# Optimization experiments

Measured on AMD Instinct MI355X. Metric: run time of the kernel, lower is better.

## Reference

```python
import jax, jax.numpy as jnp
import numpy as np

HEADS, DIM_HEAD, C, B, HS, WS = 8, 64, 512, 2, 48, 48


def setup_inputs() -> dict:
    key = jax.random.key(0)
    ks = jax.random.split(key, 9)
    s = 0.02
    return {
        "hidden_states": jax.random.normal(ks[0], (B, C, HS, WS), jnp.float32),
        "Wq": jax.random.normal(ks[1], (HEADS, DIM_HEAD, C), jnp.float32) * s,
        "bq": jax.random.normal(ks[2], (HEADS, DIM_HEAD), jnp.float32) * s,
        "Wk": jax.random.normal(ks[3], (HEADS, DIM_HEAD, C), jnp.float32) * s,
        "bk": jax.random.normal(ks[4], (HEADS, DIM_HEAD), jnp.float32) * s,
        "Wv": jax.random.normal(ks[5], (HEADS, DIM_HEAD, C), jnp.float32) * s,
        "bv": jax.random.normal(ks[6], (HEADS, DIM_HEAD), jnp.float32) * s,
        "Wo": jax.random.normal(ks[7], (C, HEADS * DIM_HEAD), jnp.float32) * s,
        "bo": jax.random.normal(ks[8], (C,), jnp.float32) * s,
    }


def reference(hidden_states, Wq, bq, Wk, bk, Wv, bv, Wo, bo):
    # hidden_states: [B, C, H, W]; per-head 1x1 convs == per-head linear over C.
    b, c, h, w = hidden_states.shape
    hw = h * w
    x = hidden_states.reshape(b, c, hw)  # [B, C, HW]
    # Batched per-head projections (fuses the per-head Conv2d loop).
    q = jnp.einsum('bcs,ndc->bnsd', x, Wq) + bq[None, :, None, :]  # [B, n, HW, d]
    k = jnp.einsum('bcs,ndc->bnsd', x, Wk) + bk[None, :, None, :]
    v = jnp.einsum('bcs,ndc->bnsd', x, Wv) + bv[None, :, None, :]
    scale = 1.0 / jnp.sqrt(jnp.asarray(DIM_HEAD, hidden_states.dtype))
    scores = jnp.einsum('bnqd,bnkd->bnqk', q, k) * scale  # [B, n, HW, HW]
    probs = jax.nn.softmax(scores, axis=-1)
    attn = jnp.einsum('bnqk,bnkd->bnqd', probs, v)  # [B, n, HW, d]
    # concat heads along last dim (matches torch.cat(..., dim=-1))
    attn = attn.transpose(0, 2, 1, 3).reshape(b, hw, HEADS * DIM_HEAD)
    out = attn @ Wo.T + bo  # [B, HW, C] (to_out[0]; to_out[1] dropout = identity)
    out = out.reshape(b, h, w, c).transpose(0, 3, 1, 2)  # [B, C, H, W]
    return out
```

## Files before the change

### kernel.cpp

```cpp
#include <hip/hip_runtime.h>
#include <hip/hip_bf16.h>

#define HEADS 8
#define DHEAD 64
#define CDIM  512
#define SEQ   2304
#define ND    512

typedef unsigned short u16;
typedef unsigned int   u32;
typedef __attribute__((ext_vector_type(8))) short short8;
typedef __attribute__((ext_vector_type(4))) float f32x4;

#define QSCALE 0.18033688011112043f

__device__ __forceinline__ u16 f2bf(float f) {
    union { float f; u32 u; } x; x.f = f;
    u32 r = x.u + 0x7FFFu + ((x.u >> 16) & 1u);
    return (u16)(r >> 16);
}
__device__ __forceinline__ float bf2f(u16 v) {
    union { u32 u; float f; } x; x.u = ((u32)v) << 16; return x.f;
}
__device__ __forceinline__ u32 pkbf(float a, float b) {
    union { float f; u32 u; } x, y; x.f = a; y.f = b;
    return __builtin_amdgcn_perm(y.u + 0x8000u, x.u + 0x8000u, 0x07060302u);
}
__device__ __forceinline__ f32x4 mfma16(short8 a, short8 b, f32x4 c) {
    return __builtin_amdgcn_mfma_f32_16x16x32_bf16(a, b, c, 0, 0, 0);
}
__device__ __forceinline__ void cp16(const void* g, void* l) {
    __builtin_amdgcn_global_load_lds(
        (const __attribute__((address_space(1))) u32*)(uintptr_t)g,
        (__attribute__((address_space(3))) u32*)(u32)(uintptr_t)l,
        16, 0, 0);
}
__device__ __forceinline__ int kperm_inv(int r) {
    return (r & ~0x1C) | ((r & 0x0C) << 1) | ((r & 0x10) >> 2);
}

__global__ void prep_kernel(const float* __restrict__ H,
                            const float* __restrict__ Wq, const float* __restrict__ Wk,
                            const float* __restrict__ Wv, const float* __restrict__ Wo,
                            u16* __restrict__ Wqkv, u16* __restrict__ Wob,
                            u16* __restrict__ X) {
    __shared__ float tile[32][33];
    const int t = threadIdx.x;
    const int bx = blockIdx.x;
    if (bx < 4096) {
        int idx = bx * 256 + t;
        const int N1 = CDIM * ND;
        if (idx < N1)             Wqkv[idx] = f2bf(Wq[idx]);
        else if (idx < 2 * N1)    Wqkv[idx] = f2bf(Wk[idx - N1]);
        else if (idx < 3 * N1)    Wqkv[idx] = f2bf(Wv[idx - 2 * N1]);
        else                      Wob[idx - 3 * N1] = f2bf(Wo[idx - 3 * N1]);
    } else {
        int bb = bx - 4096;
        int st = bb % 72, ct = (bb / 72) % 16, b = bb / (72 * 16);
        int tx = t & 31, ty = t >> 5;
#pragma unroll
        for (int k = 0; k < 4; ++k) {
            int c = ct * 32 + ty + k * 8;
            tile[ty + k * 8][tx] = H[((size_t)b * CDIM + c) * SEQ + st * 32 + tx];
        }
        __syncthreads();
#pragma unroll
        for (int k = 0; k < 4; ++k) {
            int s = st * 32 + ty + k * 8;
            X[((size_t)b * SEQ + s) * CDIM + ct * 32 + tx] = f2bf(tile[tx][ty + k * 8]);
        }
    }
}

__global__ __launch_bounds__(256) void gemm_qkv_kernel(
        const u16* __restrict__ W, const u16* __restrict__ X,
        const float* __restrict__ bq, const float* __restrict__ bk, const float* __restrict__ bv,
        u16* __restrict__ Q, u16* __restrict__ K, u16* __restrict__ V) {
    __shared__ __align__(16) u16 As[128 * 64];
    __shared__ __align__(16) u16 Bs[128 * 64];
    const int n0 = blockIdx.x * 128;
    const int m0 = blockIdx.y * 128;
    const int b  = blockIdx.z;
    const int t = threadIdx.x;
    const int lane = t & 63, w = t >> 6;
    const int l16 = lane & 15, quad = lane >> 4;
    const int wm = (w >> 1) * 64, wn = (w & 1) * 64;
    const int srow = t >> 3, scol = (t & 7) * 8;
    const u16* Xb = X + (size_t)b * SEQ * CDIM;

    f32x4 acc[4][4] = {};

    for (int kb = 0; kb < 512; kb += 64) {
        __syncthreads();
#pragma unroll
        for (int it = 0; it < 4; ++it) {
            int r2 = it * 32 + srow;
            cp16(&W [(size_t)(m0 + r2) * 512 + kb + scol], &As[r2 * 64 + scol]);
            cp16(&Xb[(size_t)(n0 + r2) * 512 + kb + scol], &Bs[r2 * 64 + scol]);
        }
        __syncthreads();
#pragma unroll
        for (int kk = 0; kk < 2; ++kk) {
            short8 af[4], bfr[4];
#pragma unroll
            for (int i = 0; i < 4; ++i)
                af[i] = *(const short8*)&As[(wm + i * 16 + l16) * 64 + kk * 32 + quad * 8];
#pragma unroll
            for (int j = 0; j < 4; ++j)
                bfr[j] = *(const short8*)&Bs[(wn + j * 16 + l16) * 64 + kk * 32 + quad * 8];
#pragma unroll
            for (int i = 0; i < 4; ++i)
#pragma unroll
                for (int j = 0; j < 4; ++j)
                    acc[i][j] = mfma16(af[i], bfr[j], acc[i][j]);
        }
    }

    if (m0 < 1024) {
        const bool isQ = (m0 < 512);
        const float* bias = isQ ? bq : bk;
        const float sc = isQ ? QSCALE : 1.0f;
        const int mq = isQ ? m0 : m0 - 512;
        u16* dst = isQ ? Q : K;
#pragma unroll
        for (int j = 0; j < 4; ++j) {
            int s = n0 + wn + j * 16 + l16;
#pragma unroll
            for (int i = 0; i < 4; ++i) {
                int mm = mq + wm + i * 16 + quad * 4;
                uint2 val;
                val.x = pkbf((acc[i][j][0] + bias[mm + 0]) * sc, (acc[i][j][1] + bias[mm + 1]) * sc);
                val.y = pkbf((acc[i][j][2] + bias[mm + 2]) * sc, (acc[i][j][3] + bias[mm + 3]) * sc);
                *(uint2*)&dst[(((size_t)(b * 8 + (mm >> 6))) * SEQ + s) * 64 + (mm & 63)] = val;
            }
        }
    } else {
#pragma unroll
        for (int j = 0; j < 4; ++j) {
            int s = n0 + wn + j * 16 + l16;
#pragma unroll
            for (int i = 0; i < 4; ++i) {
                int mbase = m0 - 1024 + wm + i * 16 + quad * 4;
#pragma unroll
                for (int r = 0; r < 4; ++r) {
                    int mm = mbase + r;
                    V[((size_t)(b * 512 + mm)) * SEQ + s] = f2bf(acc[i][j][r] + bv[mm]);
                }
            }
        }
    }
}

__global__ __launch_bounds__(256) void attn_partial(
        const u16* __restrict__ Q,
        const u16* __restrict__ K,
        const u16* __restrict__ Vt,
        u16* __restrict__ Opart,
        float* __restrict__ Lpart) {
    __shared__ __align__(16) u16 sm[2 * 64 * 64];
    u16* Ks = sm;
    u16* Vs = sm + 64 * 64;
    const int pair = blockIdx.x & 15, qt = blockIdx.x >> 4;
    const int c = blockIdx.y;
    const int b = pair >> 3, h = pair & 7;
    const int t = threadIdx.x, lane = t & 63, w = t >> 6;
    const int l16 = lane & 15, quad = lane >> 4;
    const int srow = t >> 3, scol = (t & 7) * 8;
    const int kinv0 = kperm_inv(srow), kinv1 = kperm_inv(32 + srow);

    const u16* Qg = Q + ((size_t)pair * SEQ + qt * 64) * 64;
    short8 qf0 = *(const short8*)&Qg[(size_t)(w * 16 + l16) * 64 + quad * 8];
    short8 qf1 = *(const short8*)&Qg[(size_t)(w * 16 + l16) * 64 + 32 + quad * 8];

    const u16* Kg = K  + ((size_t)pair * SEQ + c * 576) * 64;
    const u16* Vg = Vt + ((size_t)(b * 512 + h * 64)) * SEQ + c * 576;

    f32x4 lacc = {0.f, 0.f, 0.f, 0.f};
    f32x4 o[4] = {};

    for (int kt = 0; kt < 9; ++kt) {
        __syncthreads();
        cp16(&Kg[(size_t)(kt * 64 + kinv0) * 64 + scol], &Ks[srow * 64 + scol]);
        cp16(&Kg[(size_t)(kt * 64 + kinv1) * 64 + scol], &Ks[(32 + srow) * 64 + scol]);
        cp16(&Vg[(size_t)srow * SEQ + kt * 64 + scol],        &Vs[srow * 64 + scol]);
        cp16(&Vg[(size_t)(32 + srow) * SEQ + kt * 64 + scol], &Vs[(32 + srow) * 64 + scol]);
        __syncthreads();
        f32x4 sacc[4] = {};
#pragma unroll
        for (int j = 0; j < 4; ++j) {
            short8 kf0 = *(const short8*)&Ks[(j * 16 + l16) * 64 + quad * 8];
            short8 kf1 = *(const short8*)&Ks[(j * 16 + l16) * 64 + 32 + quad * 8];
            sacc[j] = mfma16(kf0, qf0, sacc[j]);
            sacc[j] = mfma16(kf1, qf1, sacc[j]);
        }
        float p[4][4];
#pragma unroll
        for (int j = 0; j < 4; ++j)
#pragma unroll
            for (int r = 0; r < 4; ++r) {
                p[j][r] = __builtin_amdgcn_exp2f(sacc[j][r]);
                lacc[j] += p[j][r];
            }
#pragma unroll
        for (int g = 0; g < 2; ++g) {
            short8 pf;
            u32* pw = (u32*)&pf;
            pw[0] = pkbf(p[2 * g][0], p[2 * g][1]);
            pw[1] = pkbf(p[2 * g][2], p[2 * g][3]);
            pw[2] = pkbf(p[2 * g + 1][0], p[2 * g + 1][1]);
            pw[3] = pkbf(p[2 * g + 1][2], p[2 * g + 1][3]);
#pragma unroll
            for (int i = 0; i < 4; ++i) {
                short8 vf = *(const short8*)&Vs[(i * 16 + l16) * 64 + g * 32 + quad * 8];
                o[i] = mfma16(vf, pf, o[i]);
            }
        }
    }
    float lrow = lacc[0] + lacc[1] + lacc[2] + lacc[3];
    lrow += __shfl_xor(lrow, 16);
    lrow += __shfl_xor(lrow, 32);
    float inv = 1.0f / lrow;
    __syncthreads();
#pragma unroll
    for (int i = 0; i < 4; ++i) {
        uint2 pk;
        pk.x = pkbf(o[i][0] * inv, o[i][1] * inv);
        pk.y = pkbf(o[i][2] * inv, o[i][3] * inv);
        *(uint2*)&sm[(w * 16 + l16) * 72 + i * 16 + quad * 4] = pk;
    }
    if (quad == 0)
        Lpart[(size_t)(c * 16 + pair) * SEQ + qt * 64 + w * 16 + l16] = lrow;
    __syncthreads();
#pragma unroll
    for (int it = 0; it < 2; ++it) {
        int v = it * 256 + t;
        int row = v >> 3, col = (v & 7) * 8;
        *(uint4*)&Opart[(((size_t)(c * 16 + pair)) * SEQ + qt * 64 + row) * 64 + col] =
            *(const uint4*)&sm[row * 72 + col];
    }
}

__global__ __launch_bounds__(256) void attn_combine(
        const u16* __restrict__ Opart, const float* __restrict__ Lpart,
        u16* __restrict__ At) {
    const int bid = blockIdx.x;
    const int pair = bid / 144, sb = bid % 144;
    const int tid = threadIdx.x;
    const int rl = tid >> 4, dg = tid & 15;
    const int s = sb * 16 + rl;
    const int b = pair >> 3, h = pair & 7;
    float wc[4], L = 0.f;
#pragma unroll
    for (int c = 0; c < 4; ++c) {
        wc[c] = Lpart[(size_t)(c * 16 + pair) * SEQ + s];
        L += wc[c];
    }
    float invL = 1.0f / L;
    float acc[4] = {0.f, 0.f, 0.f, 0.f};
#pragma unroll
    for (int c = 0; c < 4; ++c) {
        ushort4 v = *(const ushort4*)&Opart[((size_t)(c * 16 + pair) * SEQ + s) * 64 + dg * 4];
        acc[0] += wc[c] * bf2f(v.x);
        acc[1] += wc[c] * bf2f(v.y);
        acc[2] += wc[c] * bf2f(v.z);
        acc[3] += wc[c] * bf2f(v.w);
    }
    uint2 outv;
    outv.x = pkbf(acc[0] * invL, acc[1] * invL);
    outv.y = pkbf(acc[2] * invL, acc[3] * invL);
    *(uint2*)&At[((size_t)b * SEQ + s) * ND + h * 64 + dg * 4] = outv;
}

__global__ __launch_bounds__(256) void gemm_out_kernel(
        const u16* __restrict__ Wob, const u16* __restrict__ At,
        const float* __restrict__ bo, float* __restrict__ out) {
    __shared__ __align__(16) u16 As[64 * 64];
    __shared__ __align__(16) u16 Bs[128 * 64];
    const int n0 = blockIdx.x * 128;
    const int m0 = blockIdx.y * 64;
    const int b  = blockIdx.z;
    const int t = threadIdx.x;
    const int lane = t & 63, w = t >> 6;
    const int l16 = lane & 15, quad = lane >> 4;
    const int srow = t >> 3, scol = (t & 7) * 8;
    const u16* Ab = At + (size_t)b * SEQ * ND;

    f32x4 acc[4][2] = {};

    for (int kb = 0; kb < 512; kb += 64) {
        __syncthreads();
#pragma unroll
        for (int it = 0; it < 2; ++it) {
            int r2 = it * 32 + srow;
            cp16(&Wob[(size_t)(m0 + r2) * 512 + kb + scol], &As[r2 * 64 + scol]);
        }
#pragma unroll
        for (int it = 0; it < 4; ++it) {
            int r2 = it * 32 + srow;
            cp16(&Ab[(size_t)(n0 + r2) * 512 + kb + scol], &Bs[r2 * 64 + scol]);
        }
        __syncthreads();
#pragma unroll
        for (int kk = 0; kk < 2; ++kk) {
            short8 af[4], bfr[2];
#pragma unroll
            for (int i = 0; i < 4; ++i)
                af[i] = *(const short8*)&As[(i * 16 + l16) * 64 + kk * 32 + quad * 8];
#pragma unroll
            for (int j = 0; j < 2; ++j)
                bfr[j] = *(const short8*)&Bs[(w * 32 + j * 16 + l16) * 64 + kk * 32 + quad * 8];
#pragma unroll
            for (int i = 0; i < 4; ++i)
#pragma unroll
                for (int j = 0; j < 2; ++j)
                    acc[i][j] = mfma16(af[i], bfr[j], acc[i][j]);
        }
    }
#pragma unroll
    for (int i = 0; i < 4; ++i) {
        int cbase = m0 + i * 16 + quad * 4;
#pragma unroll
        for (int j = 0; j < 2; ++j) {
            int s = n0 + w * 32 + j * 16 + l16;
#pragma unroll
            for (int r = 0; r < 4; ++r) {
                int cc = cbase + r;
                out[((size_t)(b * 512 + cc)) * SEQ + s] = acc[i][j][r] + bo[cc];
            }
        }
    }
}

extern "C" void kernel_launch(void* const* d_in, const int* in_sizes, int n_in,
                              void* d_out, int out_size, void* d_ws, size_t ws_size,
                              hipStream_t stream) {
    const float* H  = (const float*)d_in[0];
    const float* Wq = (const float*)d_in[1];
    const float* bq = (const float*)d_in[2];
    const float* Wk = (const float*)d_in[3];
    const float* bk = (const float*)d_in[4];
    const float* Wv = (const float*)d_in[5];
    const float* bv = (const float*)d_in[6];
    const float* Wo = (const float*)d_in[7];
    const float* bo = (const float*)d_in[8];
    float* out = (float*)d_out;

    u16* ws    = (u16*)d_ws;
    u16* Wqkv  = ws;
    u16* Wob   = Wqkv  + 1536 * 512;
    u16* Xbf   = Wob   + 512 * 512;
    u16* Qb    = Xbf   + 2 * SEQ * CDIM;
    u16* Kb    = Qb    + 2 * SEQ * ND;
    u16* Vb    = Kb    + 2 * SEQ * ND;
    u16* At    = Vb    + 2 * SEQ * ND;
    u16* Opart = At    + 2 * SEQ * ND;
    float* Lpart = (float*)(Opart + 4 * 16 * SEQ * 64);

    prep_kernel<<<6400, 256, 0, stream>>>(H, Wq, Wk, Wv, Wo, Wqkv, Wob, Xbf);
    gemm_qkv_kernel<<<dim3(18, 12, 2), 256, 0, stream>>>(Wqkv, Xbf, bq, bk, bv, Qb, Kb, Vb);
    attn_partial<<<dim3(576, 4), 256, 0, stream>>>(Qb, Kb, Vb, Opart, Lpart);
    attn_combine<<<2304, 256, 0, stream>>>(Opart, Lpart, At);
    gemm_out_kernel<<<dim3(18, 8, 2), 256, 0, stream>>>(Wob, At, bo, out);
}
```

Measured before the change: 158.5 us.

## Swizzle LDS tiles to avoid bank conflicts and process two query tiles per attention block

Applies an XOR swizzle to the column chunk when copying tiles into shared memory in the QKV GEMM, output GEMM and attention kernel, with matching swizzled reads, to cut LDS bank conflicts on row-strided fragment loads. The attention kernel now handles 128 query rows per block, sharing each loaded K/V tile between two query sub-tiles and halving the grid. This doubles register use for accumulators and halves the block count, which may reduce occupancy and parallelism.

```diff
diff --git a/kernel.cpp b/kernel.cpp
--- a/kernel.cpp
+++ b/kernel.cpp
@@ -84,8 +84,10 @@
     const int t = threadIdx.x;
     const int lane = t & 63, w = t >> 6;
     const int l16 = lane & 15, quad = lane >> 4;
+    const int x7 = l16 & 7;
     const int wm = (w >> 1) * 64, wn = (w & 1) * 64;
     const int srow = t >> 3, scol = (t & 7) * 8;
+    const int scol_sw = ((t & 7) ^ (srow & 7)) * 8;
     const u16* Xb = X + (size_t)b * SEQ * CDIM;
 
     f32x4 acc[4][4] = {};
@@ -95,19 +97,20 @@
 #pragma unroll
         for (int it = 0; it < 4; ++it) {
             int r2 = it * 32 + srow;
-            cp16(&W [(size_t)(m0 + r2) * 512 + kb + scol], &As[r2 * 64 + scol]);
-            cp16(&Xb[(size_t)(n0 + r2) * 512 + kb + scol], &Bs[r2 * 64 + scol]);
+            cp16(&W [(size_t)(m0 + r2) * 512 + kb + scol_sw], &As[r2 * 64 + scol]);
+            cp16(&Xb[(size_t)(n0 + r2) * 512 + kb + scol_sw], &Bs[r2 * 64 + scol]);
         }
         __syncthreads();
 #pragma unroll
         for (int kk = 0; kk < 2; ++kk) {
+            const int co = ((kk * 4 + quad) ^ x7) * 8;
             short8 af[4], bfr[4];
 #pragma unroll
             for (int i = 0; i < 4; ++i)
-                af[i] = *(const short8*)&As[(wm + i * 16 + l16) * 64 + kk * 32 + quad * 8];
+                af[i] = *(const short8*)&As[(wm + i * 16 + l16) * 64 + co];
 #pragma unroll
             for (int j = 0; j < 4; ++j)
-                bfr[j] = *(const short8*)&Bs[(wn + j * 16 + l16) * 64 + kk * 32 + quad * 8];
+                bfr[j] = *(const short8*)&Bs[(wn + j * 16 + l16) * 64 + co];
 #pragma unroll
             for (int i = 0; i < 4; ++i)
 #pragma unroll
@@ -165,78 +168,114 @@
     const int b = pair >> 3, h = pair & 7;
     const int t = threadIdx.x, lane = t & 63, w = t >> 6;
     const int l16 = lane & 15, quad = lane >> 4;
-    const int srow = t >> 3, scol = (t & 7) * 8;
+    const int x7 = l16 & 7;
+    const int srow = t >> 3;
+    const int scol = (t & 7) * 8;
+    const int scol_sw = ((t & 7) ^ (srow & 7)) * 8;
     const int kinv0 = kperm_inv(srow), kinv1 = kperm_inv(32 + srow);
-
-    const u16* Qg = Q + ((size_t)pair * SEQ + qt * 64) * 64;
-    short8 qf0 = *(const short8*)&Qg[(size_t)(w * 16 + l16) * 64 + quad * 8];
-    short8 qf1 = *(const short8*)&Qg[(size_t)(w * 16 + l16) * 64 + 32 + quad * 8];
+    const int cA = (quad ^ x7) * 8;
+    const int cB = (quad ^ x7 ^ 4) * 8;
+
+    const u16* Qg = Q + ((size_t)pair * SEQ + qt * 128) * 64;
+    const int rA = w * 16 + l16, rB = 64 + rA;
+    short8 qfa0 = *(const short8*)&Qg[(size_t)rA * 64 + quad * 8];
+    short8 qfa1 = *(const short8*)&Qg[(size_t)rA * 64 + 32 + quad * 8];
+    short8 qfb0 = *(const short8*)&Qg[(size_t)rB * 64 + quad * 8];
+    short8 qfb1 = *(const short8*)&Qg[(size_t)rB * 64 + 32 + quad * 8];
 
     const u16* Kg = K  + ((size_t)pair * SEQ + c * 576) * 64;
     const u16* Vg = Vt + ((size_t)(b * 512 + h * 64)) * SEQ + c * 576;
 
-    f32x4 lacc = {0.f, 0.f, 0.f, 0.f};
-    f32x4 o[4] = {};
+    f32x4 laccA = {0.f, 0.f, 0.f, 0.f}, laccB = {0.f, 0.f, 0.f, 0.f};
+    f32x4 oA[4] = {}, oB[4] = {};
 
     for (int kt = 0; kt < 9; ++kt) {
         __syncthreads();
-        cp16(&Kg[(size_t)(kt * 64 + kinv0) * 64 + scol], &Ks[srow * 64 + scol]);
-        cp16(&Kg[(size_t)(kt * 64 + kinv1) * 64 + scol], &Ks[(32 + srow) * 64 + scol]);
-        cp16(&Vg[(size_t)srow * SEQ + kt * 64 + scol],        &Vs[srow * 64 + scol]);
-        cp16(&Vg[(size_t)(32 + srow) * SEQ + kt * 64 + scol], &Vs[(32 + srow) * 64 + scol]);
-        __syncthreads();
-        f32x4 sacc[4] = {};
+        cp16(&Kg[(size_t)(kt * 64 + kinv0) * 64 + scol_sw], &Ks[srow * 64 + scol]);
+        cp16(&Kg[(size_t)(kt * 64 + kinv1) * 64 + scol_sw], &Ks[(32 + srow) * 64 + scol]);
+        cp16(&Vg[(size_t)srow * SEQ + kt * 64 + scol_sw],        &Vs[srow * 64 + scol]);
+        cp16(&Vg[(size_t)(32 + srow) * SEQ + kt * 64 + scol_sw], &Vs[(32 + srow) * 64 + scol]);
+        __syncthreads();
+        f32x4 saccA[4] = {}, saccB[4] = {};
 #pragma unroll
         for (int j = 0; j < 4; ++j) {
-            short8 kf0 = *(const short8*)&Ks[(j * 16 + l16) * 64 + quad * 8];
-            short8 kf1 = *(const short8*)&Ks[(j * 16 + l16) * 64 + 32 + quad * 8];
-            sacc[j] = mfma16(kf0, qf0, sacc[j]);
-            sacc[j] = mfma16(kf1, qf1, sacc[j]);
-        }
-        float p[4][4];
+            short8 kf0 = *(const short8*)&Ks[(j * 16 + l16) * 64 + cA];
+            short8 kf1 = *(const short8*)&Ks[(j * 16 + l16) * 64 + cB];
+            saccA[j] = mfma16(kf0, qfa0, saccA[j]);
+            saccA[j] = mfma16(kf1, qfa1, saccA[j]);
+            saccB[j] = mfma16(kf0, qfb0, saccB[j]);
+            saccB[j] = mfma16(kf1, qfb1, saccB[j]);
+        }
+        float pA[4][4], pB[4][4];
 #pragma unroll
         for (int j = 0; j < 4; ++j)
 #pragma unroll
             for (int r = 0; r < 4; ++r) {
-                p[j][r] = __builtin_amdgcn_exp2f(sacc[j][r]);
-                lacc[j] += p[j][r];
+                pA[j][r] = __builtin_amdgcn_exp2f(saccA[j][r]);
+                laccA[j] += pA[j][r];
+                pB[j][r] = __builtin_amdgcn_exp2f(saccB[j][r]);
+                laccB[j] += pB[j][r];
             }
 #pragma unroll
         for (int g = 0; g < 2; ++g) {
-            short8 pf;
-            u32* pw = (u32*)&pf;
-            pw[0] = pkbf(p[2 * g][0], p[2 * g][1]);
-            pw[1] = pkbf(p[2 * g][2], p[2 * g][3]);
-            pw[2] = pkbf(p[2 * g + 1][0], p[2 * g + 1][1]);
-            pw[3] = pkbf(p[2 * g + 1][2], p[2 * g + 1][3]);
+            short8 pfA, pfB;
+            u32* pwA = (u32*)&pfA;
+            u32* pwB = (u32*)&pfB;
+            pwA[0] = pkbf(pA[2 * g][0], pA[2 * g][1]);
+            pwA[1] = pkbf(pA[2 * g][2], pA[2 * g][3]);
+            pwA[2] = pkbf(pA[2 * g + 1][0], pA[2 * g + 1][1]);
+            pwA[3] = pkbf(pA[2 * g + 1][2], pA[2 * g + 1][3]);
+            pwB[0] = pkbf(pB[2 * g][0], pB[2 * g][1]);
+            pwB[1] = pkbf(pB[2 * g][2], pB[2 * g][3]);
+            pwB[2] = pkbf(pB[2 * g + 1][0], pB[2 * g + 1][1]);
+            pwB[3] = pkbf(pB[2 * g + 1][2], pB[2 * g + 1][3]);
+            const int cg = g ? cB : cA;
 #pragma unroll
             for (int i = 0; i < 4; ++i) {
-                short8 vf = *(const short8*)&Vs[(i * 16 + l16) * 64 + g * 32 + quad * 8];
-                o[i] = mfma16(vf, pf, o[i]);
+                short8 vf = *(const short8*)&Vs[(i * 16 + l16) * 64 + cg];
+                oA[i] = mfma16(vf, pfA, oA[i]);
+                oB[i] = mfma16(vf, pfB, oB[i]);
             }
         }
     }
-    float lrow = lacc[0] + lacc[1] + lacc[2] + lacc[3];
-    lrow += __shfl_xor(lrow, 16);
-    lrow += __shfl_xor(lrow, 32);
-    float inv = 1.0f / lrow;
+    float lA = laccA[0] + laccA[1] + laccA[2] + laccA[3];
+    lA += __shfl_xor(lA, 16); lA += __shfl_xor(lA, 32);
+    float lB = laccB[0] + laccB[1] + laccB[2] + laccB[3];
+    lB += __shfl_xor(lB, 16); lB += __shfl_xor(lB, 32);
+    float invA = 1.0f / lA, invB = 1.0f / lB;
+    const size_t orow = ((size_t)(c * 16 + pair)) * SEQ + qt * 128;
+
     __syncthreads();
 #pragma unroll
     for (int i = 0; i < 4; ++i) {
         uint2 pk;
-        pk.x = pkbf(o[i][0] * inv, o[i][1] * inv);
-        pk.y = pkbf(o[i][2] * inv, o[i][3] * inv);
+        pk.x = pkbf(oA[i][0] * invA, oA[i][1] * invA);
+        pk.y = pkbf(oA[i][2] * invA, oA[i][3] * invA);
         *(uint2*)&sm[(w * 16 + l16) * 72 + i * 16 + quad * 4] = pk;
     }
-    if (quad == 0)
-        Lpart[(size_t)(c * 16 + pair) * SEQ + qt * 64 + w * 16 + l16] = lrow;
+    if (quad == 0) Lpart[orow + w * 16 + l16] = lA;
     __syncthreads();
 #pragma unroll
     for (int it = 0; it < 2; ++it) {
         int v = it * 256 + t;
         int row = v >> 3, col = (v & 7) * 8;
-        *(uint4*)&Opart[(((size_t)(c * 16 + pair)) * SEQ + qt * 64 + row) * 64 + col] =
-            *(const uint4*)&sm[row * 72 + col];
+        *(uint4*)&Opart[(orow + row) * 64 + col] = *(const uint4*)&sm[row * 72 + col];
+    }
+    __syncthreads();
+#pragma unroll
+    for (int i = 0; i < 4; ++i) {
+        uint2 pk;
+        pk.x = pkbf(oB[i][0] * invB, oB[i][1] * invB);
+        pk.y = pkbf(oB[i][2] * invB, oB[i][3] * invB);
+        *(uint2*)&sm[(w * 16 + l16) * 72 + i * 16 + quad * 4] = pk;
+    }
+    if (quad == 0) Lpart[orow + 64 + w * 16 + l16] = lB;
+    __syncthreads();
+#pragma unroll
+    for (int it = 0; it < 2; ++it) {
+        int v = it * 256 + t;
+        int row = v >> 3, col = (v & 7) * 8;
+        *(uint4*)&Opart[(orow + 64 + row) * 64 + col] = *(const uint4*)&sm[row * 72 + col];
     }
 }
 
@@ -282,7 +321,9 @@
     const int t = threadIdx.x;
     const int lane = t & 63, w = t >> 6;
     const int l16 = lane & 15, quad = lane >> 4;
+    const int x7 = l16 & 7;
     const int srow = t >> 3, scol = (t & 7) * 8;
+    const int scol_sw = ((t & 7) ^ (srow & 7)) * 8;
     const u16* Ab = At + (size_t)b * SEQ * ND;
 
     f32x4 acc[4][2] = {};
@@ -292,23 +333,24 @@
 #pragma unroll
         for (int it = 0; it < 2; ++it) {
             int r2 = it * 32 + srow;
-            cp16(&Wob[(size_t)(m0 + r2) * 512 + kb + scol], &As[r2 * 64 + scol]);
+            cp16(&Wob[(size_t)(m0 + r2) * 512 + kb + scol_sw], &As[r2 * 64 + scol]);
         }
 #pragma unroll
         for (int it = 0; it < 4; ++it) {
             int r2 = it * 32 + srow;
-            cp16(&Ab[(size_t)(n0 + r2) * 512 + kb + scol], &Bs[r2 * 64 + scol]);
+            cp16(&Ab[(size_t)(n0 + r2) * 512 + kb + scol_sw], &Bs[r2 * 64 + scol]);
         }
         __syncthreads();
 #pragma unroll
         for (int kk = 0; kk < 2; ++kk) {
+            const int co = ((kk * 4 + quad) ^ x7) * 8;
             short8 af[4], bfr[2];
 #pragma unroll
             for (int i = 0; i < 4; ++i)
-                af[i] = *(const short8*)&As[(i * 16 + l16) * 64 + kk * 32 + quad * 8];
+                af[i] = *(const short8*)&As[(i * 16 + l16) * 64 + co];
 #pragma unroll
             for (int j = 0; j < 2; ++j)
-                bfr[j] = *(const short8*)&Bs[(w * 32 + j * 16 + l16) * 64 + kk * 32 + quad * 8];
+                bfr[j] = *(const short8*)&Bs[(w * 32 + j * 16 + l16) * 64 + co];
 #pragma unroll
             for (int i = 0; i < 4; ++i)
 #pragma unroll
@@ -358,7 +400,7 @@
 
     prep_kernel<<<6400, 256, 0, stream>>>(H, Wq, Wk, Wv, Wo, Wqkv, Wob, Xbf);
     gemm_qkv_kernel<<<dim3(18, 12, 2), 256, 0, stream>>>(Wqkv, Xbf, bq, bk, bv, Qb, Kb, Vb);
-    attn_partial<<<dim3(576, 4), 256, 0, stream>>>(Qb, Kb, Vb, Opart, Lpart);
+    attn_partial<<<dim3(288, 4), 256, 0, stream>>>(Qb, Kb, Vb, Opart, Lpart);
     attn_combine<<<2304, 256, 0, stream>>>(Opart, Lpart, At);
     gemm_out_kernel<<<dim3(18, 8, 2), 256, 0, stream>>>(Wob, At, bo, out);
 }
```

Result: faster. 140.2 us (-11.5%).
